# Performance work log

Measured on AMD Instinct MI355X. Metric: run time of the kernel, lower is better.

Reference implementation:

```python
import jax, jax.numpy as jnp
import numpy as np

EPS = 1e-5
PI = 3.1415927410125732
B, C, N = 32, 3, 4096


def setup_inputs() -> dict:
    key = jax.random.key(0)
    ks = jax.random.split(key, 16)
    rn = lambda k, shape, scale: (jax.random.normal(k, shape, jnp.float32) * scale)
    z = lambda n: jnp.zeros((n,), jnp.float32)
    o = lambda n: jnp.ones((n,), jnp.float32)
    return {
        "x": jax.random.normal(ks[0], (B, C, N), jnp.float32),
        # conv1x1 weights stored as [out, in] (Conv1d kernel size 1)
        "w1": rn(ks[1], (64, C), 0.5), "b1": z(64), "g1": o(64), "be1": z(64),
        "w2": rn(ks[2], (128, 64), 0.12), "b2": z(128), "g2": o(128), "be2": z(128),
        "w3": rn(ks[3], (1024, 128), 0.09), "b3": z(1024), "g3": o(1024), "be3": z(1024),
        "fw1": rn(ks[4], (512, 1024), 0.03), "fb1": z(512), "g4": o(512), "be4": z(512),
        "fw2": rn(ks[5], (256, 512), 0.044), "fb2": z(256), "g5": o(256), "be5": z(256),
        "fw3": rn(ks[6], (128, 256), 0.0625), "fb3": z(128), "g6": o(128), "be6": z(128),
        "fw4": rn(ks[7], (3, 128), 0.088), "fb4": z(3),
    }


def _bn_cn(h, g, b):
    # BatchNorm1d on [B, C, N]: stats over (batch, spatial), biased variance (train mode)
    m = h.mean((0, 2), keepdims=True)
    v = ((h - m) ** 2).mean((0, 2), keepdims=True)
    return g[None, :, None] * (h - m) * jax.lax.rsqrt(v + EPS) + b[None, :, None]


def _bn_fc(h, g, b):
    # BatchNorm1d on [B, C]: stats over batch
    m = h.mean(0, keepdims=True)
    v = ((h - m) ** 2).mean(0, keepdims=True)
    return g * (h - m) * jax.lax.rsqrt(v + EPS) + b


def _euler_to_rot(ang):
    # ang: [B, 3] = (rx, ry, rz);  R = Rz @ Ry @ Rx per sample
    a, b, c = ang[:, 0], ang[:, 1], ang[:, 2]
    ca, sa = jnp.cos(a), jnp.sin(a)
    cb, sb = jnp.cos(b), jnp.sin(b)
    cc, sc = jnp.cos(c), jnp.sin(c)
    one = jnp.ones_like(a); zero = jnp.zeros_like(a)
    Rx = jnp.stack([jnp.stack([one, zero, zero], -1),
                    jnp.stack([zero, ca, -sa], -1),
                    jnp.stack([zero, sa, ca], -1)], -2)
    Ry = jnp.stack([jnp.stack([cb, zero, sb], -1),
                    jnp.stack([zero, one, zero], -1),
                    jnp.stack([-sb, zero, cb], -1)], -2)
    Rz = jnp.stack([jnp.stack([cc, -sc, zero], -1),
                    jnp.stack([sc, cc, zero], -1),
                    jnp.stack([zero, zero, one], -1)], -2)
    return jnp.matmul(Rz, jnp.matmul(Ry, Rx))  # [B, 3, 3]


def reference(x, w1, b1, g1, be1, w2, b2, g2, be2, w3, b3, g3, be3,
              fw1, fb1, g4, be4, fw2, fb2, g5, be5, fw3, fb3, g6, be6, fw4, fb4):
    h = jax.nn.relu(_bn_cn(jnp.einsum('bcn,oc->bon', x, w1) + b1[None, :, None], g1, be1))
    h = jax.nn.relu(_bn_cn(jnp.einsum('bcn,oc->bon', h, w2) + b2[None, :, None], g2, be2))
    h = jax.nn.relu(_bn_cn(jnp.einsum('bcn,oc->bon', h, w3) + b3[None, :, None], g3, be3))
    h = h.max(axis=2)  # global max pool -> [B, 1024]
    h = jax.nn.relu(_bn_fc(h @ fw1.T + fb1, g4, be4))
    h = jax.nn.relu(_bn_fc(h @ fw2.T + fb2, g5, be5))
    h = jax.nn.relu(_bn_fc(h @ fw3.T + fb3, g6, be6))
    ang = (h @ fw4.T + fb4) * PI  # [B, 3] Euler angles
    return _euler_to_rot(ang)
```

## Files before the change

### kernel.cpp

```cpp
#include <hip/hip_runtime.h>
#include <math.h>


#define EPS 1e-5f
#define PI_F 3.1415927410125732f

typedef unsigned int u32;
typedef unsigned short u16;
typedef _Float16 f16;
typedef __bf16 bf16x8 __attribute__((ext_vector_type(8)));
typedef f16 f16x8 __attribute__((ext_vector_type(8)));
typedef float f32x4 __attribute__((ext_vector_type(4)));
typedef float f32x16 __attribute__((ext_vector_type(16)));

#define AS1 __attribute__((address_space(1)))
#define AS3 __attribute__((address_space(3)))

__device__ __forceinline__ u16 f2bf(float f) {
  u32 u = __float_as_uint(f);
  return (u16)((u + 0x7FFFu + ((u >> 16) & 1u)) >> 16);
}
__device__ __forceinline__ float bf2f(u16 h) { return __uint_as_float(((u32)h) << 16); }
__device__ __forceinline__ u16 f2h(float f) {
  f16 h = (f16)f;
  union { f16 x; u16 u; } c; c.x = h; return c.u;
}
__device__ __forceinline__ u32 encf(float f) {
  u32 u = __float_as_uint(f);
  return (u & 0x80000000u) ? ~u : (u | 0x80000000u);
}
__device__ __forceinline__ float decf(u32 u) {
  return __uint_as_float((u & 0x80000000u) ? (u ^ 0x80000000u) : ~u);
}

__global__ __launch_bounds__(256) void kA_xpart(const float* __restrict__ x,
    float* __restrict__ xst_part) {
  __shared__ float wsum[4][9];
  int t = threadIdx.x;
  int tg = blockIdx.x * 256 + t;
  int b = tg >> 10, nq = (tg & 1023) << 2;
  const float* xb = x + ((size_t)b * 3) * 4096 + nq;
  float4 a = *(const float4*)(xb);
  float4 c = *(const float4*)(xb + 4096);
  float4 d = *(const float4*)(xb + 8192);
  float p[9];
  p[0] = (a.x + a.y) + (a.z + a.w);
  p[1] = (c.x + c.y) + (c.z + c.w);
  p[2] = (d.x + d.y) + (d.z + d.w);
  p[3] = fmaf(a.x,a.x, fmaf(a.y,a.y, fmaf(a.z,a.z, a.w*a.w)));
  p[4] = fmaf(a.x,c.x, fmaf(a.y,c.y, fmaf(a.z,c.z, a.w*c.w)));
  p[5] = fmaf(a.x,d.x, fmaf(a.y,d.y, fmaf(a.z,d.z, a.w*d.w)));
  p[6] = fmaf(c.x,c.x, fmaf(c.y,c.y, fmaf(c.z,c.z, c.w*c.w)));
  p[7] = fmaf(c.x,d.x, fmaf(c.y,d.y, fmaf(c.z,d.z, c.w*d.w)));
  p[8] = fmaf(d.x,d.x, fmaf(d.y,d.y, fmaf(d.z,d.z, d.w*d.w)));
  #pragma unroll
  for (int k = 0; k < 9; ++k) {
    #pragma unroll
    for (int s = 1; s < 64; s <<= 1) p[k] += __shfl_xor(p[k], s);
  }
  if ((t & 63) == 0) {
    #pragma unroll
    for (int k = 0; k < 9; ++k) wsum[t >> 6][k] = p[k];
  }
  __syncthreads();
  if (t < 9) xst_part[blockIdx.x*9 + t] = wsum[0][t] + wsum[1][t] + wsum[2][t] + wsum[3][t];
}

__global__ __launch_bounds__(256) void kC2_gram(const float* __restrict__ x,
    const float* __restrict__ xst_part,
    const float* __restrict__ w1, const float* __restrict__ b1,
    const float* __restrict__ g1, const float* __restrict__ be1,
    float* __restrict__ gram, float* __restrict__ w1f_g, float* __restrict__ b1f_g) {
  __shared__ float xsl[3][1024];
  __shared__ float4 w1s4[64];
  __shared__ __align__(16) char hfrag[4352];
  __shared__ __align__(16) char lfrag[4352];
  __shared__ float mred[256];
  __shared__ float xstL[9];
  int t = threadIdx.x, bi = blockIdx.x;
  int lane = t & 63, wid = t >> 6;
  if (t < 9) { float s = 0.f; for (int p = 0; p < 128; ++p) s += xst_part[p*9 + t]; xstL[t] = s; }
  int b = bi >> 2, n0 = (bi & 3) << 10;
  for (int i = t; i < 3072; i += 256) {
    int c = i >> 10, n = i & 1023;
    xsl[c][n] = x[((size_t)b*3 + c)*4096 + n0 + n];
  }
  __syncthreads();
  if (t < 64) {
    const float inv = 1.f/131072.f;
    float mx = xstL[0]*inv, my = xstL[1]*inv, mz = xstL[2]*inv;
    float cxx = xstL[3]*inv - mx*mx, cxy = xstL[4]*inv - mx*my, cxz = xstL[5]*inv - mx*mz;
    float cyy = xstL[6]*inv - my*my, cyz = xstL[7]*inv - my*mz, czz = xstL[8]*inv - mz*mz;
    float wa = w1[t*3], wb = w1[t*3+1], wc = w1[t*3+2];
    float mu = fmaf(wa, mx, fmaf(wb, my, fmaf(wc, mz, b1[t])));
    float var = wa*wa*cxx + wb*wb*cyy + wc*wc*czz
              + 2.f*(wa*wb*cxy + wa*wc*cxz + wb*wc*cyz);
    float s = g1[t] * rsqrtf(var + EPS);
    float bf = be1[t] + s*(b1[t] - mu);
    w1s4[t] = make_float4(s*wa, s*wb, s*wc, bf);
    if (bi == 0) { w1f_g[t*3] = s*wa; w1f_g[t*3+1] = s*wb; w1f_g[t*3+2] = s*wc; b1f_g[t] = bf; }
  }
  __syncthreads();
  int ch = t & 63, ptg = t >> 6;
  float4 wv = w1s4[ch];
  int wbyte = (ch >> 4)*1088 + (((ch & 15) | (ptg << 4)) << 4);
  const f32x4 zero4 = {0.f,0.f,0.f,0.f};
  f32x4 acc[4] = {zero4, zero4, zero4, zero4};
  float msum = 0.f;
  for (int it = 0; it < 32; ++it) {
    int p0 = (it << 5) | (ptg << 3);
    u32 hw[4], lw[4];
    #pragma unroll
    for (int q = 0; q < 4; ++q) {
      int pA = p0 + 2*q, pB = p0 + 2*q + 1;
      float v0 = fmaxf(fmaf(wv.x, xsl[0][pA], fmaf(wv.y, xsl[1][pA], fmaf(wv.z, xsl[2][pA], wv.w))), 0.f);
      float v1 = fmaxf(fmaf(wv.x, xsl[0][pB], fmaf(wv.y, xsl[1][pB], fmaf(wv.z, xsl[2][pB], wv.w))), 0.f);
      msum += v0 + v1;
      u16 h0 = f2bf(v0), h1 = f2bf(v1);
      hw[q] = (u32)h0 | ((u32)h1 << 16);
      lw[q] = (u32)f2bf(v0 - bf2f(h0)) | ((u32)f2bf(v1 - bf2f(h1)) << 16);
    }
    *(uint4*)(hfrag + wbyte) = make_uint4(hw[0],hw[1],hw[2],hw[3]);
    *(uint4*)(lfrag + wbyte) = make_uint4(lw[0],lw[1],lw[2],lw[3]);
    __syncthreads();
    bf16x8 ah = *(const bf16x8*)(hfrag + wid*1088 + (lane << 4));
    bf16x8 al = *(const bf16x8*)(lfrag + wid*1088 + (lane << 4));
    #pragma unroll
    for (int cg2 = 0; cg2 < 4; ++cg2) {
      bf16x8 bh = *(const bf16x8*)(hfrag + cg2*1088 + (lane << 4));
      bf16x8 bl = *(const bf16x8*)(lfrag + cg2*1088 + (lane << 4));
      acc[cg2] = __builtin_amdgcn_mfma_f32_16x16x32_bf16(al, bh, acc[cg2], 0, 0, 0);
      acc[cg2] = __builtin_amdgcn_mfma_f32_16x16x32_bf16(ah, bl, acc[cg2], 0, 0, 0);
      acc[cg2] = __builtin_amdgcn_mfma_f32_16x16x32_bf16(ah, bh, acc[cg2], 0, 0, 0);
    }
    __syncthreads();
  }
  mred[t] = msum;
  __syncthreads();
  if (t < 64)
    atomicAdd(&gram[4096 + t], mred[t] + mred[t+64] + mred[t+128] + mred[t+192]);
  #pragma unroll
  for (int cg2 = 0; cg2 < 4; ++cg2) {
    #pragma unroll
    for (int r = 0; r < 4; ++r) {
      int i = (wid << 4) | (((lane >> 4) << 2) | r);
      int j = (cg2 << 4) | (lane & 15);
      atomicAdd(&gram[i*64 + j], acc[cg2][r]);
    }
  }
}

__global__ __launch_bounds__(64) void kD_fold2(const float* __restrict__ gram,
    const float* __restrict__ w2, const float* __restrict__ b2,
    const float* __restrict__ g2, const float* __restrict__ be2,
    float* __restrict__ w2f, float* __restrict__ b2f) {
  __shared__ float wrow[64];
  int o = blockIdx.x, i = threadIdx.x;
  wrow[i] = w2[o*64 + i];
  __syncthreads();
  float si = 0.f;
  #pragma unroll 8
  for (int j = 0; j < 64; ++j) si = fmaf(wrow[j], gram[j*64 + i], si);
  const float inv = 1.f / 131072.f;
  float qi = wrow[i] * si;
  float di = wrow[i] * (gram[4096 + i] * inv);
  #pragma unroll
  for (int d2 = 1; d2 < 64; d2 <<= 1) { qi += __shfl_xor(qi, d2); di += __shfl_xor(di, d2); }
  float mu2 = di + b2[o];
  float var = qi*inv - di*di;
  float s = g2[o] * rsqrtf(var + EPS);
  w2f[o*64 + i] = s * wrow[i];
  if (i == 0) b2f[o] = be2[o] + s*(b2[o] - mu2);
}

__global__ __launch_bounds__(256) void kE2_layer2(const float* __restrict__ x,
    const float* __restrict__ w1f, const float* __restrict__ b1f,
    const float* __restrict__ w2f, const float* __restrict__ b2f,
    u16* __restrict__ h2t) {
  __shared__ float xs[3][256];
  __shared__ float4 w1s4[64];
  __shared__ __align__(16) char h1h[17408];
  __shared__ __align__(16) char h1l[17408];
  int t = threadIdx.x;
  int b = ((blockIdx.x & 7) << 2) | ((blockIdx.x >> 3) & 3);
  int ntile = (blockIdx.x >> 5) << 8;
  int lane = t & 63, wid = t >> 6;
  int wo = wid & 1, wn = wid >> 1;
  #pragma unroll
  for (int i = 0; i < 3; ++i) {
    int idx = (i << 8) | t;
    int c = idx >> 8, n = idx & 255;
    xs[c][n] = x[((size_t)b*3 + c)*4096 + ntile + n];
  }
  if (t < 64) w1s4[t] = make_float4(w1f[t*3], w1f[t*3+1], w1f[t*3+2], b1f[t]);
  bf16x8 wf_hi[4][2], wf_lo[4][2];
  float4 bvv[4];
  #pragma unroll
  for (int of = 0; of < 4; ++of) {
    int o2r = (wo << 6) | (of << 4) | (lane & 15);
    bvv[of] = *(const float4*)(b2f + (wo << 6) + (of << 4) + ((lane >> 4) << 2));
    #pragma unroll
    for (int ks1 = 0; ks1 < 2; ++ks1) {
      const float* src = w2f + o2r*64 + (ks1 << 5) + ((lane >> 4) << 3);
      float4 f0 = *(const float4*)src;
      float4 f1 = *(const float4*)(src + 4);
      float fv[8] = {f0.x,f0.y,f0.z,f0.w, f1.x,f1.y,f1.z,f1.w};
      u32 hw[4], lw[4];
      #pragma unroll
      for (int p2 = 0; p2 < 4; ++p2) {
        u16 h0 = f2bf(fv[2*p2]), h1 = f2bf(fv[2*p2+1]);
        u16 l0 = f2bf(fv[2*p2] - bf2f(h0)), l1 = f2bf(fv[2*p2+1] - bf2f(h1));
        hw[p2] = (u32)h0 | ((u32)h1 << 16);
        lw[p2] = (u32)l0 | ((u32)l1 << 16);
      }
      uint4 H = make_uint4(hw[0],hw[1],hw[2],hw[3]);
      uint4 L = make_uint4(lw[0],lw[1],lw[2],lw[3]);
      wf_hi[of][ks1] = *(const bf16x8*)&H;
      wf_lo[of][ks1] = *(const bf16x8*)&L;
    }
  }
  __syncthreads();
  const f32x4 zero4 = {0.f,0.f,0.f,0.f};
  for (int chunk = 0; chunk < 2; ++chunk) {
    {
      int n = t >> 1, ks1 = t & 1;
      int nL = (chunk << 7) | n;
      float xa = xs[0][nL], xb = xs[1][nL], xc = xs[2][nL];
      int fb = (((n >> 4) << 1) | ks1) * 1088 + ((n & 15) << 4);
      #pragma unroll
      for (int kq = 0; kq < 4; ++kq) {
        u32 hw[4], lw[4];
        #pragma unroll
        for (int p2 = 0; p2 < 4; ++p2) {
          int k1 = (ks1 << 5) | (kq << 3) | (p2 << 1);
          float4 wv0 = w1s4[k1];
          float4 wv1 = w1s4[k1 + 1];
          float v0 = fmaxf(fmaf(wv0.x, xa, fmaf(wv0.y, xb, fmaf(wv0.z, xc, wv0.w))), 0.f);
          float v1 = fmaxf(fmaf(wv1.x, xa, fmaf(wv1.y, xb, fmaf(wv1.z, xc, wv1.w))), 0.f);
          u16 h0 = f2bf(v0), h1_ = f2bf(v1);
          hw[p2] = (u32)h0 | ((u32)h1_ << 16);
          lw[p2] = (u32)f2bf(v0 - bf2f(h0)) | ((u32)f2bf(v1 - bf2f(h1_)) << 16);
        }
        *(uint4*)(h1h + fb + (kq << 8)) = make_uint4(hw[0],hw[1],hw[2],hw[3]);
        *(uint4*)(h1l + fb + (kq << 8)) = make_uint4(lw[0],lw[1],lw[2],lw[3]);
      }
    }
    __syncthreads();
    #pragma unroll
    for (int nb = 0; nb < 4; ++nb) {
      int fbase = (((wn << 2) | nb) << 1) * 1088 + (lane << 4);
      bf16x8 bh0 = *(const bf16x8*)(h1h + fbase);
      bf16x8 bh1 = *(const bf16x8*)(h1h + fbase + 1088);
      bf16x8 bl0 = *(const bf16x8*)(h1l + fbase);
      bf16x8 bl1 = *(const bf16x8*)(h1l + fbase + 1088);
      int nblk_g = (ntile >> 4) | (chunk << 3) | (wn << 2) | nb;
      #pragma unroll
      for (int of = 0; of < 4; ++of) {
        f32x4 acc;
        acc = __builtin_amdgcn_mfma_f32_16x16x32_bf16(wf_hi[of][0], bl0, zero4, 0, 0, 0);
        acc = __builtin_amdgcn_mfma_f32_16x16x32_bf16(wf_lo[of][0], bh0, acc, 0, 0, 0);
        acc = __builtin_amdgcn_mfma_f32_16x16x32_bf16(wf_hi[of][0], bh0, acc, 0, 0, 0);
        acc = __builtin_amdgcn_mfma_f32_16x16x32_bf16(wf_hi[of][1], bl1, acc, 0, 0, 0);
        acc = __builtin_amdgcn_mfma_f32_16x16x32_bf16(wf_lo[of][1], bh1, acc, 0, 0, 0);
        acc = __builtin_amdgcn_mfma_f32_16x16x32_bf16(wf_hi[of][1], bh1, acc, 0, 0, 0);
        ushort4 hs;
        hs.x = f2h(fmaxf(acc[0] + bvv[of].x, 0.f));
        hs.y = f2h(fmaxf(acc[1] + bvv[of].y, 0.f));
        hs.z = f2h(fmaxf(acc[2] + bvv[of].z, 0.f));
        hs.w = f2h(fmaxf(acc[3] + bvv[of].w, 0.f));
        int ks2 = (wo << 1) | (of >> 1);
        int q = ((of & 1) << 1) | ((lane >> 5) & 1);
        int l = (lane & 15) | (q << 4);
        int j0 = ((lane >> 4) & 1) << 2;
        size_t idx = ((((size_t)((b << 8) | nblk_g) << 2) | ks2) << 9) + (l << 3) + j0;
        *(ushort4*)(h2t + idx) = hs;
      }
    }
    __syncthreads();
  }
}

__global__ __launch_bounds__(256, 2) void k5_layer3(
    const u16* __restrict__ h2t, const float* __restrict__ w3,
    float* __restrict__ sum3, float* __restrict__ sq3,
    u32* __restrict__ maxe, u32* __restrict__ mine) {
  __shared__ __align__(16) char smem[65536];
  const int t = threadIdx.x, lane = t & 63, wid = t >> 6;
  const int id = blockIdx.x;
  const int xcd = id & 7, rest = id >> 3;
  const int gq = rest & 15, otile = rest >> 4;
  const int g = (gq << 3) | xcd;
  const int b = g >> 2, q = g & 3;

  const size_t gbase = ((size_t)b << 19) | ((size_t)q << 17);
  auto STAGE = [&](int c, int buf) {
    char* lb = smem + buf * 32768;
    size_t gb = gbase + ((size_t)c << 14);
    #pragma unroll
    for (int i = 0; i < 8; ++i) {
      int off = (i << 12) | (t << 4);
      __builtin_amdgcn_global_load_lds((const AS1 u32*)(h2t + gb + (off >> 1)),
          (AS3 u32*)(lb + off), 16, 0, 0);
    }
  };
  STAGE(0, 0); STAGE(1, 1);

  f16x8 wh[8], wl[8];
  {
    int o3 = (otile << 7) | (wid << 5) | (lane & 31);
    #pragma unroll
    for (int ks = 0; ks < 8; ++ks) {
      const float* src = w3 + (size_t)o3*128 + (ks << 4) + ((lane >> 5) << 3);
      float4 f0 = *(const float4*)src;
      float4 f1 = *(const float4*)(src + 4);
      float fv[8] = {f0.x,f0.y,f0.z,f0.w, f1.x,f1.y,f1.z,f1.w};
      f16x8 vh, vl;
      #pragma unroll
      for (int p2 = 0; p2 < 8; ++p2) {
        f16 hh = (f16)fv[p2];
        vh[p2] = hh;
        vl[p2] = (f16)(fv[p2] - (float)hh);
      }
      wh[ks] = vh;
      wl[ks] = vl;
    }
  }

  const int aoff = (((lane >> 4) & 1) << 12) | ((((lane & 15) | (((lane >> 5) & 1) << 4))) << 4);

  const f32x16 zero16 = {0.f,0.f,0.f,0.f,0.f,0.f,0.f,0.f,0.f,0.f,0.f,0.f,0.f,0.f,0.f,0.f};
  float rs = 0.f, rq = 0.f, rmx = -3.4e38f, rmn = 3.4e38f;

  for (int c = 0; c < 8; ++c) {
    if (c < 7) asm volatile("s_waitcnt vmcnt(8)" ::: "memory");
    else       asm volatile("s_waitcnt vmcnt(0)" ::: "memory");
    __builtin_amdgcn_s_barrier();
    const char* bp = smem + (c & 1) * 32768 + aoff;
    __builtin_amdgcn_s_setprio(1);
    #pragma unroll
    for (int nf = 0; nf < 4; ++nf) {
      const char* bn = bp + (nf << 13);
      f32x16 accA, accB;
      #pragma unroll
      for (int ks = 0; ks < 8; ++ks) {
        int ao = ((ks >> 1) << 10) | ((ks & 1) << 9);
        f16x8 av = *(const f16x8*)(bn + ao);
        accA = __builtin_amdgcn_mfma_f32_32x32x16_f16(av, wh[ks], ks ? accA : zero16, 0, 0, 0);
        accB = __builtin_amdgcn_mfma_f32_32x32x16_f16(av, wl[ks], ks ? accB : zero16, 0, 0, 0);
      }
      f32x16 acc = accA + accB;
      #pragma unroll
      for (int r = 0; r < 16; r += 4) {
        rs += ((acc[r] + acc[r+1]) + (acc[r+2] + acc[r+3]));
        rq = fmaf(acc[r],acc[r], fmaf(acc[r+1],acc[r+1],
             fmaf(acc[r+2],acc[r+2], fmaf(acc[r+3],acc[r+3], rq))));
        rmx = fmaxf(fmaxf(rmx, fmaxf(acc[r],acc[r+1])), fmaxf(acc[r+2],acc[r+3]));
        rmn = fminf(fminf(rmn, fminf(acc[r],acc[r+1])), fminf(acc[r+2],acc[r+3]));
      }
    }
    __builtin_amdgcn_s_setprio(0);
    __builtin_amdgcn_s_barrier();
    if (c < 6) STAGE(c + 2, c & 1);
  }

  rs += __shfl_xor(rs, 32);
  rq += __shfl_xor(rq, 32);
  rmx = fmaxf(rmx, __shfl_xor(rmx, 32));
  rmn = fminf(rmn, __shfl_xor(rmn, 32));
  if (lane < 32) {
    int go = (b << 10) | (otile << 7) | (wid << 5) | lane;
    atomicAdd(&sum3[go], rs);
    atomicAdd(&sq3[go], rq);
    atomicMax(&maxe[go], encf(rmx));
    atomicMin(&mine[go], encf(rmn));
  }
}

__global__ void k_fin3_pool(const float* __restrict__ sum3, const float* __restrict__ sq3,
    const u32* __restrict__ maxe, const u32* __restrict__ mine,
    const float* __restrict__ b3,
    const float* __restrict__ g, const float* __restrict__ be, float* __restrict__ pool) {
  int o = blockIdx.x*256 + threadIdx.x;
  float S = 0.f, Q = 0.f;
  for (int b = 0; b < 32; ++b) { S += sum3[(b<<10)|o]; Q += sq3[(b<<10)|o]; }
  const float inv = 1.f/131072.f;
  float ma = S*inv;
  float m = ma + b3[o];
  float var = Q*inv - ma*ma;
  float sc = g[o]*rsqrtf(var + EPS);
  float sh = be[o] - sc*m;
  bool pos = (sc >= 0.f);
  for (int b = 0; b < 32; ++b) {
    float v = decf(pos ? maxe[(b<<10)|o] : mine[(b<<10)|o]) + b3[o];
    pool[(b<<10)|o] = fmaxf(fmaf(sc, v, sh), 0.f);
  }
}

__global__ __launch_bounds__(256) void k_fc_bn_relu(const float* __restrict__ in,
    const float* __restrict__ w, const float* __restrict__ fb,
    const float* __restrict__ g, const float* __restrict__ be,
    float* __restrict__ out, int K, int F) {
  __shared__ float wrow[1024];
  __shared__ float preb[32];
  int o = blockIdx.x, t = threadIdx.x;
  for (int k = t; k < K; k += 256) wrow[k] = w[(size_t)o*K + k];
  __syncthreads();
  int b = t >> 3, j = t & 7;
  int per = K >> 3;
  const float* inb = in + (size_t)b*K + j*per;
  const float* wp  = wrow + j*per;
  float p = 0.f;
  for (int k = 0; k < per; ++k) p = fmaf(inb[k], wp[k], p);
  p += __shfl_xor(p, 1); p += __shfl_xor(p, 2); p += __shfl_xor(p, 4);
  if (j == 0) preb[b] = p + fb[o];
  __syncthreads();
  if (t < 32) {
    float v = preb[t];
    float s = v;
    #pragma unroll
    for (int d = 1; d < 32; d <<= 1) s += __shfl_xor(s, d);
    float m = s * 0.03125f;
    float dv = v - m;
    float q = dv*dv;
    #pragma unroll
    for (int d = 1; d < 32; d <<= 1) q += __shfl_xor(q, d);
    float var = q * 0.03125f;
    float sc = g[o]*rsqrtf(var + EPS);
    out[(size_t)t*F + o] = fmaxf(fmaf(sc, dv, be[o]), 0.f);
  }
}

__global__ __launch_bounds__(128) void k_final(const float* __restrict__ h6,
    const float* __restrict__ fw4, const float* __restrict__ fb4, float* __restrict__ out) {
  __shared__ float angs[32][3];
  int t = threadIdx.x;
  if (t < 96) {
    int b = t / 3, j = t % 3;
    float p = 0.f;
    #pragma unroll 4
    for (int k = 0; k < 128; ++k) p = fmaf(h6[b*128+k], fw4[j*128+k], p);
    angs[b][j] = (p + fb4[j]) * PI_F;
  }
  __syncthreads();
  if (t < 32) {
    float a = angs[t][0], bb = angs[t][1], c = angs[t][2];
    float sa, ca; sincosf(a,  &sa, &ca);
    float sb, cb; sincosf(bb, &sb, &cb);
    float sc, cc; sincosf(c,  &sc, &cc);
    float* o9 = out + t*9;
    o9[0] = cc*cb;
    o9[1] = fmaf(cc*sb, sa, -sc*ca);
    o9[2] = fmaf(cc*sb, ca,  sc*sa);
    o9[3] = sc*cb;
    o9[4] = fmaf(sc*sb, sa,  cc*ca);
    o9[5] = fmaf(sc*sb, ca, -cc*sa);
    o9[6] = -sb;
    o9[7] = cb*sa;
    o9[8] = cb*ca;
  }
}

extern "C" void kernel_launch(void* const* d_in, const int* in_sizes, int n_in,
                              void* d_out, int out_size, void* d_ws, size_t ws_size,
                              hipStream_t stream) {
  (void)in_sizes; (void)n_in; (void)out_size; (void)ws_size;
  const float* x   = (const float*)d_in[0];
  const float* w1  = (const float*)d_in[1];
  const float* b1  = (const float*)d_in[2];
  const float* g1  = (const float*)d_in[3];
  const float* be1 = (const float*)d_in[4];
  const float* w2  = (const float*)d_in[5];
  const float* b2  = (const float*)d_in[6];
  const float* g2  = (const float*)d_in[7];
  const float* be2 = (const float*)d_in[8];
  const float* w3  = (const float*)d_in[9];
  const float* b3  = (const float*)d_in[10];
  const float* g3  = (const float*)d_in[11];
  const float* be3 = (const float*)d_in[12];
  const float* fw1 = (const float*)d_in[13];
  const float* fb1 = (const float*)d_in[14];
  const float* g4  = (const float*)d_in[15];
  const float* be4 = (const float*)d_in[16];
  const float* fw2 = (const float*)d_in[17];
  const float* fb2 = (const float*)d_in[18];
  const float* g5p = (const float*)d_in[19];
  const float* be5 = (const float*)d_in[20];
  const float* fw3 = (const float*)d_in[21];
  const float* fb3 = (const float*)d_in[22];
  const float* g6  = (const float*)d_in[23];
  const float* be6 = (const float*)d_in[24];
  const float* fw4 = (const float*)d_in[25];
  const float* fb4 = (const float*)d_in[26];

  u16* h2t = (u16*)d_ws;
  float* acc0 = (float*)d_ws + 8388608;
  float* xst_part = acc0;
  float* w1f  = acc0 + 1152;
  float* b1f  = acc0 + 1344;
  float* w2f  = acc0 + 1408;
  float* b2f  = acc0 + 9600;
  float* gram = acc0 + 9728;
  float* sum3 = acc0 + 13888;
  float* sq3  = acc0 + 46656;
  u32*   maxe = (u32*)(acc0 + 79424);
  u32*   mine = (u32*)(acc0 + 112192);
  float* pool = acc0 + 144960;
  float* h4v  = acc0 + 177728;
  float* h5v  = acc0 + 194112;
  float* h6v  = acc0 + 202304;

  hipMemsetAsync(acc0 + 9728, 0, 4160ull*4, stream);
  hipMemsetAsync(acc0 + 13888, 0, 3ull*32768*4, stream);
  hipMemsetAsync(acc0 + 112192, 0xFF, 32768ull*4, stream);

  kA_xpart<<<128, 256, 0, stream>>>(x, xst_part);
  kC2_gram<<<128, 256, 0, stream>>>(x, xst_part, w1, b1, g1, be1, gram, w1f, b1f);
  kD_fold2<<<128, 64, 0, stream>>>(gram, w2, b2, g2, be2, w2f, b2f);
  kE2_layer2<<<512, 256, 0, stream>>>(x, w1f, b1f, w2f, b2f, h2t);
  k5_layer3<<<1024, 256, 0, stream>>>(h2t, w3, sum3, sq3, maxe, mine);
  k_fin3_pool<<<4, 256, 0, stream>>>(sum3, sq3, maxe, mine, b3, g3, be3, pool);
  k_fc_bn_relu<<<512, 256, 0, stream>>>(pool, fw1, fb1, g4, be4, h4v, 1024, 512);
  k_fc_bn_relu<<<256, 256, 0, stream>>>(h4v, fw2, fb2, g5p, be5, h5v, 512, 256);
  k_fc_bn_relu<<<128, 256, 0, stream>>>(h5v, fw3, fb3, g6, be6, h6v, 256, 128);
  k_final<<<1, 128, 0, stream>>>(h6v, fw4, fb4, (float*)d_out);
}
```

Before: 168.1 us.

## Fold accumulator memsets into first kernel and fuse last FC layer with final head

Removes the three hipMemsetAsync calls by having kA_xpart zero the layer-3 sum/sq/max/min accumulators and the gram buffer, and replaces the fc3 BN-ReLU kernel plus the final kernel with a single one-block kernel that computes fc3 into shared memory and then the angles and rotation. This cuts launch and memset overhead on a latency-bound chain. In exchange fc3 now runs on a single block of 4 waves looping over 128 outputs, which serializes work that was previously spread over 128 blocks. Correctness also depends on kC2_gram, which accumulates into gram, running only after kA_xpart has zeroed it.

```diff
diff --git a/kernel.cpp b/kernel.cpp
--- a/kernel.cpp
+++ b/kernel.cpp
@@ -34,10 +34,17 @@
 }
 
 __global__ __launch_bounds__(256) void kA_xpart(const float* __restrict__ x,
-    float* __restrict__ xst_part) {
+    float* __restrict__ xst_part,
+    float* __restrict__ sum3, float* __restrict__ sq3,
+    u32* __restrict__ maxe, u32* __restrict__ mine, float* __restrict__ gram) {
   __shared__ float wsum[4][9];
   int t = threadIdx.x;
   int tg = blockIdx.x * 256 + t;
+  sum3[tg] = 0.f;
+  sq3[tg] = 0.f;
+  maxe[tg] = 0u;
+  mine[tg] = 0xFFFFFFFFu;
+  if (tg < 4160) gram[tg] = 0.f;
   int b = tg >> 10, nq = (tg & 1023) << 2;
   const float* xb = x + ((size_t)b * 3) * 4096 + nq;
   float4 a = *(const float4*)(xb);
@@ -430,16 +437,44 @@
   }
 }
 
-__global__ __launch_bounds__(128) void k_final(const float* __restrict__ h6,
-    const float* __restrict__ fw4, const float* __restrict__ fb4, float* __restrict__ out) {
+__global__ __launch_bounds__(256) void k_tail3(const float* __restrict__ h5v,
+    const float* __restrict__ fw3, const float* __restrict__ fb3,
+    const float* __restrict__ g6, const float* __restrict__ be6,
+    const float* __restrict__ fw4, const float* __restrict__ fb4,
+    float* __restrict__ out) {
+  __shared__ float h6s[32][128];
   __shared__ float angs[32][3];
-  int t = threadIdx.x;
+  int t = threadIdx.x, lane = t & 63, wid = t >> 6;
+  int b = lane >> 1, j = lane & 1;
+  for (int o0 = 0; o0 < 128; o0 += 4) {
+    int o = o0 + wid;
+    const float* inb = h5v + b*256 + j*128;
+    const float* wp  = fw3 + (size_t)o*256 + j*128;
+    float p = 0.f;
+    #pragma unroll 8
+    for (int k = 0; k < 128; ++k) p = fmaf(inb[k], wp[k], p);
+    p += __shfl_xor(p, 1);
+    float pp = p + fb3[o];
+    float v = __shfl(pp, (lane & 31) << 1);
+    float s = v;
+    #pragma unroll
+    for (int d = 1; d < 32; d <<= 1) s += __shfl_xor(s, d);
+    float m = s * 0.03125f;
+    float dv = v - m;
+    float q2 = dv*dv;
+    #pragma unroll
+    for (int d = 1; d < 32; d <<= 1) q2 += __shfl_xor(q2, d);
+    float var = q2 * 0.03125f;
+    float sc = g6[o]*rsqrtf(var + EPS);
+    if (lane < 32) h6s[lane][o] = fmaxf(fmaf(sc, dv, be6[o]), 0.f);
+  }
+  __syncthreads();
   if (t < 96) {
-    int b = t / 3, j = t % 3;
+    int bb = t / 3, jj = t % 3;
     float p = 0.f;
     #pragma unroll 4
-    for (int k = 0; k < 128; ++k) p = fmaf(h6[b*128+k], fw4[j*128+k], p);
-    angs[b][j] = (p + fb4[j]) * PI_F;
+    for (int k = 0; k < 128; ++k) p = fmaf(h6s[bb][k], fw4[jj*128 + k], p);
+    angs[bb][jj] = (p + fb4[jj]) * PI_F;
   }
   __syncthreads();
   if (t < 32) {
@@ -507,13 +542,8 @@
   float* pool = acc0 + 144960;
   float* h4v  = acc0 + 177728;
   float* h5v  = acc0 + 194112;
-  float* h6v  = acc0 + 202304;
-
-  hipMemsetAsync(acc0 + 9728, 0, 4160ull*4, stream);
-  hipMemsetAsync(acc0 + 13888, 0, 3ull*32768*4, stream);
-  hipMemsetAsync(acc0 + 112192, 0xFF, 32768ull*4, stream);
-
-  kA_xpart<<<128, 256, 0, stream>>>(x, xst_part);
+
+  kA_xpart<<<128, 256, 0, stream>>>(x, xst_part, sum3, sq3, maxe, mine, gram);
   kC2_gram<<<128, 256, 0, stream>>>(x, xst_part, w1, b1, g1, be1, gram, w1f, b1f);
   kD_fold2<<<128, 64, 0, stream>>>(gram, w2, b2, g2, be2, w2f, b2f);
   kE2_layer2<<<512, 256, 0, stream>>>(x, w1f, b1f, w2f, b2f, h2t);
@@ -521,6 +551,5 @@
   k_fin3_pool<<<4, 256, 0, stream>>>(sum3, sq3, maxe, mine, b3, g3, be3, pool);
   k_fc_bn_relu<<<512, 256, 0, stream>>>(pool, fw1, fb1, g4, be4, h4v, 1024, 512);
   k_fc_bn_relu<<<256, 256, 0, stream>>>(h4v, fw2, fb2, g5p, be5, h5v, 512, 256);
-  k_fc_bn_relu<<<128, 256, 0, stream>>>(h5v, fw3, fb3, g6, be6, h6v, 256, 128);
-  k_final<<<1, 128, 0, stream>>>(h6v, fw4, fb4, (float*)d_out);
-}
+  k_tail3<<<1, 256, 0, stream>>>(h5v, fw3, fb3, g6, be6, fw4, fb4, (float*)d_out);
+}
```

Measured after the change: 343.6 us. +104.4%, slower.
